# Performance work log

Hardware: AMD Instinct MI355X
Metric: run time of the kernel (lower is better)

Reference implementation:

```python
import jax, jax.numpy as jnp
import numpy as np

B, S, H, FF, E = 4, 4096, 1024, 4096, 8
EPS = 1e-5


def setup_inputs() -> dict:
    key = jax.random.key(0)
    ks = jax.random.split(key, 8)
    std = 0.02
    return {
        "x": jax.random.normal(ks[0], (B, S, H), jnp.float32),
        "norm_weight": jnp.ones((H,), jnp.float32),
        "router_w": jax.random.normal(ks[1], (E, H), jnp.float32) * std,
        "router_b": jnp.zeros((E,), jnp.float32),
        "fc1_w": jax.random.normal(ks[2], (E, FF, H), jnp.float32) * std,
        "fc1_b": jnp.zeros((E, FF), jnp.float32),
        "fc2_w": jax.random.normal(ks[3], (E, H, FF), jnp.float32) * std,
        "fc2_b": jnp.zeros((E, H), jnp.float32),
    }


def reference(x, norm_weight, router_w, router_b, fc1_w, fc1_b, fc2_w, fc2_b):
    b, s, h = x.shape
    T = b * s
    e = router_w.shape[0]
    cap = T // e  # expert capacity, capacity_factor = 1.0

    x_flat = x.reshape(T, h)
    # RMSNorm (pre-norm on MoE input)
    xn = x_flat * jax.lax.rsqrt(jnp.mean(x_flat * x_flat, axis=-1, keepdims=True) + EPS) * norm_weight

    # Router (no jitter: eval / jitter_noise=0)
    logits = xn @ router_w.T + router_b          # [T, E]
    probs = jax.nn.softmax(logits, axis=-1)       # [T, E]

    # Expert-choice routing: each expert picks its top-`cap` tokens by prob
    gates, idx = jax.lax.top_k(probs.T, cap)      # [E, cap], [E, cap]

    # Dispatch (gather) and grouped expert MLP
    xe = xn[idx]                                   # [E, cap, H]
    hmid = jnp.einsum('ech,efh->ecf', xe, fc1_w) + fc1_b[:, None, :]
    hmid = jax.nn.gelu(hmid, approximate=False)    # torch F.gelu default (exact)
    ye = jnp.einsum('ecf,ehf->ech', hmid, fc2_w) + fc2_b[:, None, :]

    # Combine: gated scatter-add back to token positions, normalize by gate sum
    flat_idx = idx.reshape(-1)                     # [E*cap]
    weighted = (ye * gates[..., None]).reshape(-1, h)
    out = jnp.zeros((T, h), x.dtype).at[flat_idx].add(weighted)
    gate_sums = jnp.zeros((T, 1), x.dtype).at[flat_idx].add(gates.reshape(-1, 1))
    out = out / jnp.maximum(gate_sums, 1e-9)       # unrouted tokens stay zero
    return out.reshape(b, s, h)
```

## Files before the change

### kernel.cpp

```cpp
#include <hip/hip_runtime.h>
#include <hip/hip_bf16.h>

#define T_TOK 16384
#define H_DIM 1024
#define FF_DIM 4096
#define NE 8
#define CAP 2048
#define EPS_F 1e-5f

#define BM2 256
#define BN2 256
#define BK2 32

typedef __attribute__((ext_vector_type(4))) float f32x4;
typedef __attribute__((ext_vector_type(8))) short bf16x8;
typedef unsigned long long u64;
typedef unsigned int u32;

__device__ inline void gload_lds16(const void* g, void* l) {
  __builtin_amdgcn_global_load_lds(
      (const __attribute__((address_space(1))) unsigned int*)g,
      (__attribute__((address_space(3))) unsigned int*)l, 16, 0, 0);
}

__device__ inline unsigned short bf16_bits(float f) {
  __hip_bfloat16 h = __float2bfloat16(f);
  unsigned short u;
  __builtin_memcpy(&u, &h, 2);
  return u;
}

__device__ inline float bits_f32(unsigned short u) {
  const u32 x = ((u32)u) << 16;
  float f;
  __builtin_memcpy(&f, &x, 4);
  return f;
}

__global__ __launch_bounds__(256) void router_kernel(
    const float* __restrict__ x, const float* __restrict__ nw,
    const float* __restrict__ rw, const float* __restrict__ rb,
    __hip_bfloat16* __restrict__ xn, u64* __restrict__ keys) {
  const int t = blockIdx.x;
  const int tid = threadIdx.x;
  const float4 v = reinterpret_cast<const float4*>(x + (size_t)t * H_DIM)[tid];
  float ss = v.x * v.x + v.y * v.y + v.z * v.z + v.w * v.w;
#pragma unroll
  for (int o = 32; o > 0; o >>= 1) ss += __shfl_down(ss, o);
  __shared__ float red[4];
  __shared__ float redl[4][NE];
  const int wv = tid >> 6, ln = tid & 63;
  if (ln == 0) red[wv] = ss;
  __syncthreads();
  const float tot = red[0] + red[1] + red[2] + red[3];
  const float scale = rsqrtf(tot * (1.0f / H_DIM) + EPS_F);
  const float4 w4 = reinterpret_cast<const float4*>(nw)[tid];
  float xv0 = v.x * scale * w4.x, xv1 = v.y * scale * w4.y;
  float xv2 = v.z * scale * w4.z, xv3 = v.w * scale * w4.w;
  ushort4 u4;
  u4.x = bf16_bits(xv0); u4.y = bf16_bits(xv1);
  u4.z = bf16_bits(xv2); u4.w = bf16_bits(xv3);
  reinterpret_cast<ushort4*>(xn + (size_t)t * H_DIM)[tid] = u4;
  float lg[NE];
#pragma unroll
  for (int e = 0; e < NE; ++e) {
    const float4 r4 = reinterpret_cast<const float4*>(rw + (size_t)e * H_DIM)[tid];
    lg[e] = xv0 * r4.x + xv1 * r4.y + xv2 * r4.z + xv3 * r4.w;
  }
#pragma unroll
  for (int o = 32; o > 0; o >>= 1) {
#pragma unroll
    for (int e = 0; e < NE; ++e) lg[e] += __shfl_down(lg[e], o);
  }
  if (ln == 0) {
#pragma unroll
    for (int e = 0; e < NE; ++e) redl[wv][e] = lg[e];
  }
  __syncthreads();
  if (tid == 0) {
    float l[NE];
    float m = -1e30f;
#pragma unroll
    for (int e = 0; e < NE; ++e) {
      l[e] = redl[0][e] + redl[1][e] + redl[2][e] + redl[3][e] + rb[e];
      m = fmaxf(m, l[e]);
    }
    float s = 0.f;
#pragma unroll
    for (int e = 0; e < NE; ++e) { l[e] = expf(l[e] - m); s += l[e]; }
    const float inv = 1.0f / s;
#pragma unroll
    for (int e = 0; e < NE; ++e) {
      const float p = l[e] * inv;
      const u64 key = ((u64)__float_as_uint(p) << 32) | (u32)(0xFFFFFFFFu - (u32)t);
      keys[(size_t)e * T_TOK + t] = key;
    }
  }
}

#define EQCAP 7168
__global__ __launch_bounds__(1024) void topk_kernel(
    const u64* __restrict__ keys, int* __restrict__ idxl,
    float* __restrict__ gatel, int* __restrict__ tok_list, int* __restrict__ tok_cnt) {
  const int e = blockIdx.x;
  const int tid = threadIdx.x;
  const int lane = tid & 63;
  const u64* ke = keys + (size_t)e * T_TOK;
  __shared__ int hist[256];
  __shared__ u32 s_pref;
  __shared__ int s_k;
  __shared__ int s_cnt;
  __shared__ int s_eq;
  __shared__ u32 eqlist[EQCAP];

  u32 pref = 0;
  int pbits = 0;
  int kneed = CAP;
  for (int pass = 0; pass < 4; ++pass) {
    if (tid < 256) hist[tid] = 0;
    __syncthreads();
    const int shift = 24 - 8 * pass;
    for (int i = tid; i < T_TOK; i += 1024) {
      const u32 hi = (u32)(ke[i] >> 32);
      const bool ok = (pbits == 0) || ((hi >> (32 - pbits)) == pref);
      const int d = ok ? (int)((hi >> shift) & 255) : -1;
      u64 act = __ballot(ok);
      while (act) {
        const int src = __ffsll((long long)act) - 1;
        const int dl = __shfl(d, src);
        const u64 mb = __ballot(ok && (d == dl));
        if (lane == src) atomicAdd(&hist[dl], (int)__popcll(mb));
        act &= ~mb;
      }
    }
    __syncthreads();
    if (tid == 0) {
      int cum = 0;
      int d = 255;
      for (; d >= 0; --d) {
        cum += hist[d];
        if (cum >= kneed) break;
      }
      s_k = kneed - (cum - hist[d]);
      s_pref = (pref << 8) | (u32)d;
    }
    __syncthreads();
    pref = s_pref;
    kneed = s_k;
    pbits += 8;
    __syncthreads();
  }
  const u32 thrp = pref;
  const float thrp_f = __uint_as_float(thrp);

  if (tid == 0) { s_cnt = 0; s_eq = 0; }
  __syncthreads();
  for (int i = tid; i < T_TOK; i += 1024) {
    const u64 key = ke[i];
    const u32 hi = (u32)(key >> 32);
    if (hi > thrp) {
      const int pos = atomicAdd(&s_cnt, 1);
      if (pos < CAP) {
        const int tok = (int)(0xFFFFFFFFu - (u32)key);
        idxl[e * CAP + pos] = tok;
        gatel[e * CAP + pos] = __uint_as_float(hi);
        const int j = atomicAdd(tok_cnt + tok, 1);
        if (j < NE) tok_list[tok * NE + j] = e * CAP + pos;
      }
    } else if (hi == thrp) {
      const int j = atomicAdd(&s_eq, 1);
      if (j < EQCAP) eqlist[j] = (u32)key;
    }
  }
  __syncthreads();
  const int neq = s_eq;
  if (neq <= EQCAP) {
    u32 prefl = 0;
    int pb = 0;
    int kn = kneed;
    if (neq > kneed) {
      for (int pass = 0; pass < 4; ++pass) {
        if (tid < 256) hist[tid] = 0;
        __syncthreads();
        const int shift = 24 - 8 * pass;
        for (int i = tid; i < neq; i += 1024) {
          const u32 vv = eqlist[i];
          if ((pb == 0) || ((vv >> (32 - pb)) == prefl)) atomicAdd(&hist[(vv >> shift) & 255], 1);
        }
        __syncthreads();
        if (tid == 0) {
          int cum = 0;
          int d = 255;
          for (; d >= 0; --d) {
            cum += hist[d];
            if (cum >= kn) break;
          }
          s_k = kn - (cum - hist[d]);
          s_pref = (prefl << 8) | (u32)d;
        }
        __syncthreads();
        prefl = s_pref;
        kn = s_k;
        pb += 8;
        __syncthreads();
      }
    }
    for (int i = tid; i < neq; i += 1024) {
      const u32 lo = eqlist[i];
      if (neq <= kneed || lo >= prefl) {
        const int pos = atomicAdd(&s_cnt, 1);
        if (pos < CAP) {
          const int tok = (int)(0xFFFFFFFFu - lo);
          idxl[e * CAP + pos] = tok;
          gatel[e * CAP + pos] = thrp_f;
          const int j = atomicAdd(tok_cnt + tok, 1);
          if (j < NE) tok_list[tok * NE + j] = e * CAP + pos;
        }
      }
    }
  } else {
    u64 pref64 = (u64)thrp;
    int pb64 = 32;
    int kn = kneed;
    for (int pass = 4; pass < 8; ++pass) {
      if (tid < 256) hist[tid] = 0;
      __syncthreads();
      const int shift = 56 - 8 * pass;
      for (int i = tid; i < T_TOK; i += 1024) {
        const u64 key = ke[i];
        if ((key >> (64 - pb64)) == pref64) atomicAdd(&hist[(int)((key >> shift) & 255)], 1);
      }
      __syncthreads();
      if (tid == 0) {
        int cum = 0;
        int d = 255;
        for (; d >= 0; --d) {
          cum += hist[d];
          if (cum >= kn) break;
        }
        s_k = kn - (cum - hist[d]);
        s_pref = (u32)d;
      }
      __syncthreads();
      pref64 = (pref64 << 8) | s_pref;
      kn = s_k;
      pb64 += 8;
      __syncthreads();
    }
    for (int i = tid; i < T_TOK; i += 1024) {
      const u64 key = ke[i];
      if ((u32)(key >> 32) == thrp && key >= pref64) {
        const int pos = atomicAdd(&s_cnt, 1);
        if (pos < CAP) {
          const int tok = (int)(0xFFFFFFFFu - (u32)key);
          idxl[e * CAP + pos] = tok;
          gatel[e * CAP + pos] = thrp_f;
          const int j = atomicAdd(tok_cnt + tok, 1);
          if (j < NE) tok_list[tok * NE + j] = e * CAP + pos;
        }
      }
    }
  }
}

template <int MODE>
__global__ __launch_bounds__(1024, 4) void gemm9_kernel(
    const __hip_bfloat16* __restrict__ Asrc, const float* __restrict__ Bw,
    const float* __restrict__ bias, const int* __restrict__ idxl,
    const float* __restrict__ gatel, __hip_bfloat16* __restrict__ hmid,
    __hip_bfloat16* __restrict__ ye, int ebase) {
  constexpr int N = (MODE == 0) ? FF_DIM : H_DIM;
  constexpr int K = (MODE == 0) ? H_DIM : FF_DIM;
  constexpr int NBN = N / BN2;
  constexpr int LOG_NBN = (MODE == 0) ? 4 : 2;
  constexpr int BPE = (CAP / BM2) * NBN;
  constexpr int LOG_BPE = (MODE == 0) ? 7 : 5;
  constexpr int NT = K / BK2;

  const int nwg = gridDim.x;
  const int wg0 = blockIdx.x;
  const int wg = (wg0 & 7) * (nwg >> 3) + (wg0 >> 3);
  const int z = wg >> LOG_BPE;
  const int rr = wg & (BPE - 1);
  const int bm = rr >> LOG_NBN;
  const int bn = rr & (NBN - 1);
  const int e = ebase + z;

  const int tid = threadIdx.x;
  const int lane = tid & 63;
  const int w = tid >> 6;
  const int wr = w >> 2, wc = w & 3;
  const int fr = lane & 15, q = lane >> 4;

  __shared__ char smem[147456];

  const int arow = tid >> 2;
  const int ag = tid & 3;
  const int askz = (ag ^ ((arow >> 1) & 3)) * 8;
  const __hip_bfloat16* asrc;
  if constexpr (MODE == 0) {
    const int t0 = idxl[e * CAP + bm * BM2 + arow];
    asrc = Asrc + (size_t)t0 * H_DIM + askz;
  } else {
    asrc = Asrc + ((size_t)z * CAP + bm * BM2 + arow) * FF_DIM + askz;
  }
  const int brow = tid >> 3;
  const int bg = tid & 7;
  const int bskz = (bg ^ (brow & 7)) * 4;
  const float* bsrc0 = Bw + (size_t)z * N * K + (size_t)(bn * BN2 + brow) * K + bskz;
  const float* bsrc1 = bsrc0 + (size_t)128 * K;

  f32x4 acc[4][4] = {};

#define STAGE9(sb, k0)                                   \
  do {                                                   \
    char* d_ = smem + (sb)*49152 + tid * 16;             \
    gload_lds16(asrc + (k0), d_);                        \
    gload_lds16(bsrc0 + (k0), d_ + 16384);               \
    gload_lds16(bsrc1 + (k0), d_ + 32768);               \
  } while (0)

  STAGE9(0, 0);
  STAGE9(1, BK2);
  STAGE9(2, 2 * BK2);
  asm volatile("s_waitcnt vmcnt(6)");
  __builtin_amdgcn_s_barrier();
  __builtin_amdgcn_sched_barrier(0);

  for (int kt = 0; kt < NT; ++kt) {
    const int sl = kt % 3;
    const char* base = smem + sl * 49152;
    bf16x8 Af[4], Bf[4];
#pragma unroll
    for (int m = 0; m < 4; ++m)
      Af[m] = *reinterpret_cast<const bf16x8*>(
          base + (wr * 64 + m * 16 + fr) * 64 + ((q ^ ((fr >> 1) & 3)) << 4));
#pragma unroll
    for (int n = 0; n < 4; ++n) {
      const int row = wc * 64 + n * 16 + fr;
      const char* rb = base + 16384 + row * 128;
      const float4 lo = *reinterpret_cast<const float4*>(rb + (((2 * q) ^ (row & 7)) << 4));
      const float4 hi = *reinterpret_cast<const float4*>(rb + (((2 * q + 1) ^ (row & 7)) << 4));
      bf16x8 f;
      f[0] = (short)bf16_bits(lo.x); f[1] = (short)bf16_bits(lo.y);
      f[2] = (short)bf16_bits(lo.z); f[3] = (short)bf16_bits(lo.w);
      f[4] = (short)bf16_bits(hi.x); f[5] = (short)bf16_bits(hi.y);
      f[6] = (short)bf16_bits(hi.z); f[7] = (short)bf16_bits(hi.w);
      Bf[n] = f;
    }
    asm volatile("s_waitcnt lgkmcnt(0)");
    __builtin_amdgcn_sched_barrier(0);
    __builtin_amdgcn_s_barrier();
    __builtin_amdgcn_sched_barrier(0);
    const int kref = (kt + 3 < NT) ? (kt + 3) : (kt + 3 - NT);
    STAGE9(sl, kref * BK2);
    asm volatile("s_waitcnt vmcnt(6)");
    __builtin_amdgcn_sched_barrier(0);
    __builtin_amdgcn_s_setprio(1);
#pragma unroll
    for (int m_ = 0; m_ < 4; ++m_)
#pragma unroll
      for (int n_ = 0; n_ < 4; ++n_)
        acc[m_][n_] = __builtin_amdgcn_mfma_f32_16x16x32_bf16(Af[m_], Bf[n_], acc[m_][n_], 0, 0, 0);
    __builtin_amdgcn_s_setprio(0);
    __builtin_amdgcn_s_barrier();
    __builtin_amdgcn_sched_barrier(0);
  }
#undef STAGE9

  if constexpr (MODE == 0) {
#pragma unroll
    for (int m = 0; m < 4; ++m) {
      const int rbase = bm * BM2 + wr * 64 + m * 16 + q * 4;
#pragma unroll
      for (int n = 0; n < 4; ++n) {
        const int gn = bn * BN2 + wc * 64 + n * 16 + fr;
        const float bb = bias[e * FF_DIM + gn];
#pragma unroll
        for (int i = 0; i < 4; ++i) {
          const float v = acc[m][n][i] + bb;
          const float u = v * (1.5957691216f + 0.0713548162972f * v * v);
          const float s = 1.0f / (1.0f + __expf(-u));
          hmid[((size_t)z * CAP + rbase + i) * FF_DIM + gn] = __float2bfloat16(v * s);
        }
      }
    }
  } else {
#pragma unroll
    for (int m = 0; m < 4; ++m) {
      const int rbase = bm * BM2 + wr * 64 + m * 16 + q * 4;
      float gt[4];
#pragma unroll
      for (int i = 0; i < 4; ++i) gt[i] = gatel[e * CAP + rbase + i];
#pragma unroll
      for (int n = 0; n < 4; ++n) {
        const int gn = bn * BN2 + wc * 64 + n * 16 + fr;
        const float bb = bias[e * H_DIM + gn];
#pragma unroll
        for (int i = 0; i < 4; ++i)
          ye[((size_t)e * CAP + rbase + i) * H_DIM + gn] =
              __float2bfloat16((acc[m][n][i] + bb) * gt[i]);
      }
    }
  }
}

__global__ __launch_bounds__(256) void combine_kernel(
    const __hip_bfloat16* __restrict__ ye, const float* __restrict__ gatel,
    const int* __restrict__ tok_list, const int* __restrict__ tok_cnt,
    float* __restrict__ out) {
  const int t = blockIdx.x;
  const int tid = threadIdx.x;
  const int cnt = tok_cnt[t];
  float a0 = 0.f, a1 = 0.f, a2 = 0.f, a3 = 0.f, gs = 0.f;
  for (int j = 0; j < cnt && j < NE; ++j) {
    const int ent = tok_list[t * NE + j];
    gs += gatel[ent];
    const ushort4 v = reinterpret_cast<const ushort4*>(ye + (size_t)ent * H_DIM)[tid];
    a0 += bits_f32(v.x);
    a1 += bits_f32(v.y);
    a2 += bits_f32(v.z);
    a3 += bits_f32(v.w);
  }
  const float inv = 1.0f / fmaxf(gs, 1e-9f);
  float4 o;
  o.x = a0 * inv; o.y = a1 * inv; o.z = a2 * inv; o.w = a3 * inv;
  reinterpret_cast<float4*>(out + (size_t)t * H_DIM)[tid] = o;
}

extern "C" void kernel_launch(void* const* d_in, const int* in_sizes, int n_in,
                              void* d_out, int out_size, void* d_ws, size_t ws_size,
                              hipStream_t stream) {
  const float* x = (const float*)d_in[0];
  const float* nw = (const float*)d_in[1];
  const float* rw = (const float*)d_in[2];
  const float* rb = (const float*)d_in[3];
  const float* fc1w = (const float*)d_in[4];
  const float* fc1b = (const float*)d_in[5];
  const float* fc2w = (const float*)d_in[6];
  const float* fc2b = (const float*)d_in[7];
  float* out = (float*)d_out;

  char* ws = (char*)d_ws;
  size_t off = 0;
  auto alloc = [&](size_t b) {
    char* p = ws + off;
    off += (b + 255) & ~(size_t)255;
    return p;
  };
  __hip_bfloat16* xn = (__hip_bfloat16*)alloc((size_t)T_TOK * H_DIM * 2);
  u64* keys = (u64*)alloc((size_t)NE * T_TOK * 8);
  int* idxl = (int*)alloc((size_t)NE * CAP * 4);
  float* gatel = (float*)alloc((size_t)NE * CAP * 4);
  int* tok_list = (int*)alloc((size_t)T_TOK * NE * 4);
  int* tok_cnt = (int*)alloc((size_t)T_TOK * 4);
  __hip_bfloat16* ye = (__hip_bfloat16*)alloc((size_t)NE * CAP * H_DIM * 2);

  int EC = NE;
  while (EC > 1) {
    const size_t per = (size_t)EC * (size_t)CAP * FF_DIM * 2;
    if (off + per + 4096 <= ws_size) break;
    EC >>= 1;
  }
  __hip_bfloat16* hmid = (__hip_bfloat16*)alloc((size_t)EC * CAP * FF_DIM * 2);

  hipMemsetAsync(tok_cnt, 0, (size_t)T_TOK * 4, stream);

  router_kernel<<<T_TOK, 256, 0, stream>>>(x, nw, rw, rb, xn, keys);
  topk_kernel<<<NE, 1024, 0, stream>>>(keys, idxl, gatel, tok_list, tok_cnt);

  for (int eb = 0; eb < NE; eb += EC) {
    const int nb1 = EC * (CAP / BM2) * (FF_DIM / BN2);
    gemm9_kernel<0><<<nb1, 1024, 0, stream>>>(xn, fc1w + (size_t)eb * FF_DIM * H_DIM, fc1b,
                                              idxl, gatel, hmid, ye, eb);
    const int nb2 = EC * (CAP / BM2) * (H_DIM / BN2);
    gemm9_kernel<1><<<nb2, 1024, 0, stream>>>(hmid, fc2w + (size_t)eb * H_DIM * FF_DIM, fc2b,
                                              idxl, gatel, hmid, ye, eb);
  }
  combine_kernel<<<T_TOK, 256, 0, stream>>>(ye, gatel, tok_list, tok_cnt, out);
}
```

Baseline: 629.7 us.

## Convert fp32 weights to bf16 once per tile in LDS and split MFMA phases

The GEMM main loop now reads fp32 weight rows into registers, converts them to bf16 once, and writes them into LDS. Previously every wave converted fp32 values read from LDS, duplicating the conversion work, and the fp32 staging used twice the LDS space. The loop is restructured into a 4-slot ring: A tiles arrive via direct global-to-LDS loads three tiles ahead, B tiles are register-prefetched two ahead, and the MFMA work is split into two halves around the convert-and-write step to overlap it. The token-count memset is folded into the router kernel. The pipeline adds register pressure and barrier/waitcnt subtleties that could introduce hazards.

```diff
diff --git a/kernel.cpp b/kernel.cpp
--- a/kernel.cpp
+++ b/kernel.cpp
@@ -40,9 +40,11 @@
 __global__ __launch_bounds__(256) void router_kernel(
     const float* __restrict__ x, const float* __restrict__ nw,
     const float* __restrict__ rw, const float* __restrict__ rb,
-    __hip_bfloat16* __restrict__ xn, u64* __restrict__ keys) {
+    __hip_bfloat16* __restrict__ xn, u64* __restrict__ keys,
+    int* __restrict__ tok_cnt) {
   const int t = blockIdx.x;
   const int tid = threadIdx.x;
+  if (tid == 0) tok_cnt[t] = 0;
   const float4 v = reinterpret_cast<const float4*>(x + (size_t)t * H_DIM)[tid];
   float ss = v.x * v.x + v.y * v.y + v.z * v.z + v.w * v.w;
 #pragma unroll
@@ -264,7 +266,7 @@
 }
 
 template <int MODE>
-__global__ __launch_bounds__(1024, 4) void gemm9_kernel(
+__global__ __launch_bounds__(1024) void gemm11_kernel(
     const __hip_bfloat16* __restrict__ Asrc, const float* __restrict__ Bw,
     const float* __restrict__ bias, const int* __restrict__ idxl,
     const float* __restrict__ gatel, __hip_bfloat16* __restrict__ hmid,
@@ -292,81 +294,111 @@
   const int wr = w >> 2, wc = w & 3;
   const int fr = lane & 15, q = lane >> 4;
 
-  __shared__ char smem[147456];
-
-  const int arow = tid >> 2;
-  const int ag = tid & 3;
-  const int askz = (ag ^ ((arow >> 1) & 3)) * 8;
+  __shared__ char smem[131072];
+
+  const int srow = tid >> 2;
+  const int sg = tid & 3;
+  const int skoff = (sg ^ ((srow >> 1) & 3)) * 8;
+
   const __hip_bfloat16* asrc;
   if constexpr (MODE == 0) {
-    const int t0 = idxl[e * CAP + bm * BM2 + arow];
-    asrc = Asrc + (size_t)t0 * H_DIM + askz;
+    const int t0 = idxl[e * CAP + bm * BM2 + srow];
+    asrc = Asrc + (size_t)t0 * H_DIM + skoff;
   } else {
-    asrc = Asrc + ((size_t)z * CAP + bm * BM2 + arow) * FF_DIM + askz;
-  }
-  const int brow = tid >> 3;
-  const int bg = tid & 7;
-  const int bskz = (bg ^ (brow & 7)) * 4;
-  const float* bsrc0 = Bw + (size_t)z * N * K + (size_t)(bn * BN2 + brow) * K + bskz;
-  const float* bsrc1 = bsrc0 + (size_t)128 * K;
+    asrc = Asrc + ((size_t)z * CAP + bm * BM2 + srow) * FF_DIM + skoff;
+  }
+  const float* bsrcf = Bw + (size_t)z * N * K + (size_t)(bn * BN2 + srow) * K + skoff;
+
+  const int slotk = ((q ^ ((fr >> 1) & 3)) << 4);
+  const int aoff0 = (wr * 64 + fr) * 64 + slotk;
+  const int boff0 = 16384 + (wc * 64 + fr) * 64 + slotk;
 
   f32x4 acc[4][4] = {};
-
-#define STAGE9(sb, k0)                                   \
-  do {                                                   \
-    char* d_ = smem + (sb)*49152 + tid * 16;             \
-    gload_lds16(asrc + (k0), d_);                        \
-    gload_lds16(bsrc0 + (k0), d_ + 16384);               \
-    gload_lds16(bsrc1 + (k0), d_ + 32768);               \
+  bf16x8 Af[4], Bf[4];
+  float4 bA0, bA1, bB0, bB1;
+
+#define GLDA(sb, k0) gload_lds16(asrc + (k0), smem + (sb)*32768 + tid * 16)
+#define CVT_WRITE(sl, c0, c1)                                               \
+  do {                                                                      \
+    bf16x8 wv_;                                                             \
+    wv_[0] = (short)bf16_bits((c0).x); wv_[1] = (short)bf16_bits((c0).y);   \
+    wv_[2] = (short)bf16_bits((c0).z); wv_[3] = (short)bf16_bits((c0).w);   \
+    wv_[4] = (short)bf16_bits((c1).x); wv_[5] = (short)bf16_bits((c1).y);   \
+    wv_[6] = (short)bf16_bits((c1).z); wv_[7] = (short)bf16_bits((c1).w);   \
+    *reinterpret_cast<bf16x8*>(smem + (sl)*32768 + 16384 + tid * 16) = wv_; \
   } while (0)
 
-  STAGE9(0, 0);
-  STAGE9(1, BK2);
-  STAGE9(2, 2 * BK2);
-  asm volatile("s_waitcnt vmcnt(6)");
+  GLDA(0, 0);
+  GLDA(1, BK2);
+  {
+    const float4 t0 = *reinterpret_cast<const float4*>(bsrcf);
+    const float4 t1 = *reinterpret_cast<const float4*>(bsrcf + 4);
+    CVT_WRITE(0, t0, t1);
+  }
+  __builtin_amdgcn_sched_barrier(0);
+  bA0 = *reinterpret_cast<const float4*>(bsrcf + BK2);
+  bA1 = *reinterpret_cast<const float4*>(bsrcf + BK2 + 4);
+  __builtin_amdgcn_sched_barrier(0);
+  GLDA(2, 2 * BK2);
+  __builtin_amdgcn_sched_barrier(0);
+  asm volatile("s_waitcnt lgkmcnt(0)");
   __builtin_amdgcn_s_barrier();
   __builtin_amdgcn_sched_barrier(0);
 
-  for (int kt = 0; kt < NT; ++kt) {
-    const int sl = kt % 3;
-    const char* base = smem + sl * 49152;
-    bf16x8 Af[4], Bf[4];
-#pragma unroll
-    for (int m = 0; m < 4; ++m)
-      Af[m] = *reinterpret_cast<const bf16x8*>(
-          base + (wr * 64 + m * 16 + fr) * 64 + ((q ^ ((fr >> 1) & 3)) << 4));
-#pragma unroll
-    for (int n = 0; n < 4; ++n) {
-      const int row = wc * 64 + n * 16 + fr;
-      const char* rb = base + 16384 + row * 128;
-      const float4 lo = *reinterpret_cast<const float4*>(rb + (((2 * q) ^ (row & 7)) << 4));
-      const float4 hi = *reinterpret_cast<const float4*>(rb + (((2 * q + 1) ^ (row & 7)) << 4));
-      bf16x8 f;
-      f[0] = (short)bf16_bits(lo.x); f[1] = (short)bf16_bits(lo.y);
-      f[2] = (short)bf16_bits(lo.z); f[3] = (short)bf16_bits(lo.w);
-      f[4] = (short)bf16_bits(hi.x); f[5] = (short)bf16_bits(hi.y);
-      f[6] = (short)bf16_bits(hi.z); f[7] = (short)bf16_bits(hi.w);
-      Bf[n] = f;
-    }
-    asm volatile("s_waitcnt lgkmcnt(0)");
-    __builtin_amdgcn_sched_barrier(0);
-    __builtin_amdgcn_s_barrier();
-    __builtin_amdgcn_sched_barrier(0);
-    const int kref = (kt + 3 < NT) ? (kt + 3) : (kt + 3 - NT);
-    STAGE9(sl, kref * BK2);
-    asm volatile("s_waitcnt vmcnt(6)");
-    __builtin_amdgcn_sched_barrier(0);
-    __builtin_amdgcn_s_setprio(1);
-#pragma unroll
-    for (int m_ = 0; m_ < 4; ++m_)
-#pragma unroll
-      for (int n_ = 0; n_ < 4; ++n_)
-        acc[m_][n_] = __builtin_amdgcn_mfma_f32_16x16x32_bf16(Af[m_], Bf[n_], acc[m_][n_], 0, 0, 0);
-    __builtin_amdgcn_s_setprio(0);
-    __builtin_amdgcn_s_barrier();
-    __builtin_amdgcn_sched_barrier(0);
-  }
-#undef STAGE9
+#define TILE(kt, c0, c1, n0, n1)                                                               \
+  {                                                                                            \
+    const int cur_ = (kt)&3;                                                                   \
+    const int psl_ = ((kt) + 3) & 3;                                                           \
+    const int bsl_ = ((kt) + 1) & 3;                                                           \
+    const int krA_ = ((kt) + 3 < NT) ? (kt) + 3 : (kt) + 3 - NT;                               \
+    const int krB_ = ((kt) + 2 < NT) ? (kt) + 2 : (kt) + 2 - NT;                               \
+    const char* base_ = smem + cur_ * 32768;                                                   \
+    Af[0] = *reinterpret_cast<const bf16x8*>(base_ + aoff0);                                   \
+    Af[1] = *reinterpret_cast<const bf16x8*>(base_ + aoff0 + 1024);                            \
+    Af[2] = *reinterpret_cast<const bf16x8*>(base_ + aoff0 + 2048);                            \
+    Af[3] = *reinterpret_cast<const bf16x8*>(base_ + aoff0 + 3072);                            \
+    Bf[0] = *reinterpret_cast<const bf16x8*>(base_ + boff0);                                   \
+    Bf[1] = *reinterpret_cast<const bf16x8*>(base_ + boff0 + 1024);                            \
+    __builtin_amdgcn_sched_barrier(0);                                                         \
+    Bf[2] = *reinterpret_cast<const bf16x8*>(base_ + boff0 + 2048);                            \
+    Bf[3] = *reinterpret_cast<const bf16x8*>(base_ + boff0 + 3072);                            \
+    n0 = *reinterpret_cast<const float4*>(bsrcf + krB_ * BK2);                                 \
+    n1 = *reinterpret_cast<const float4*>(bsrcf + krB_ * BK2 + 4);                             \
+    __builtin_amdgcn_sched_barrier(0);                                                         \
+    GLDA(psl_, krA_ * BK2);                                                                    \
+    __builtin_amdgcn_sched_barrier(0);                                                         \
+    asm volatile("s_waitcnt vmcnt(6)");          \
+    __builtin_amdgcn_s_barrier();                                                              \
+    asm volatile("s_waitcnt lgkmcnt(2)");                             \
+    __builtin_amdgcn_sched_barrier(0);                                                         \
+    __builtin_amdgcn_s_setprio(1);                                                             \
+    _Pragma("unroll") for (int m_ = 0; m_ < 4; ++m_) {                                         \
+      acc[m_][0] = __builtin_amdgcn_mfma_f32_16x16x32_bf16(Af[m_], Bf[0], acc[m_][0], 0, 0, 0);\
+      acc[m_][1] = __builtin_amdgcn_mfma_f32_16x16x32_bf16(Af[m_], Bf[1], acc[m_][1], 0, 0, 0);\
+    }                                                                                          \
+    __builtin_amdgcn_s_setprio(0);                                                             \
+    __builtin_amdgcn_sched_barrier(0);                                                         \
+    CVT_WRITE(bsl_, c0, c1);              \
+    asm volatile("s_waitcnt lgkmcnt(0)");                                                      \
+    __builtin_amdgcn_sched_barrier(0);                                                         \
+    __builtin_amdgcn_s_barrier();                                                              \
+    __builtin_amdgcn_sched_barrier(0);                                                         \
+    __builtin_amdgcn_s_setprio(1);                                                             \
+    _Pragma("unroll") for (int m_ = 0; m_ < 4; ++m_) {                                         \
+      acc[m_][2] = __builtin_amdgcn_mfma_f32_16x16x32_bf16(Af[m_], Bf[2], acc[m_][2], 0, 0, 0);\
+      acc[m_][3] = __builtin_amdgcn_mfma_f32_16x16x32_bf16(Af[m_], Bf[3], acc[m_][3], 0, 0, 0);\
+    }                                                                                          \
+    __builtin_amdgcn_s_setprio(0);                                                             \
+    __builtin_amdgcn_sched_barrier(0);                                                         \
+  }
+
+  for (int kt = 0; kt < NT; kt += 2) {
+    TILE(kt, bA0, bA1, bB0, bB1);
+    TILE(kt + 1, bB0, bB1, bA0, bA1);
+  }
+#undef TILE
+#undef GLDA
+#undef CVT_WRITE
 
   if constexpr (MODE == 0) {
 #pragma unroll
@@ -464,18 +496,16 @@
   }
   __hip_bfloat16* hmid = (__hip_bfloat16*)alloc((size_t)EC * CAP * FF_DIM * 2);
 
-  hipMemsetAsync(tok_cnt, 0, (size_t)T_TOK * 4, stream);
-
-  router_kernel<<<T_TOK, 256, 0, stream>>>(x, nw, rw, rb, xn, keys);
+  router_kernel<<<T_TOK, 256, 0, stream>>>(x, nw, rw, rb, xn, keys, tok_cnt);
   topk_kernel<<<NE, 1024, 0, stream>>>(keys, idxl, gatel, tok_list, tok_cnt);
 
   for (int eb = 0; eb < NE; eb += EC) {
     const int nb1 = EC * (CAP / BM2) * (FF_DIM / BN2);
-    gemm9_kernel<0><<<nb1, 1024, 0, stream>>>(xn, fc1w + (size_t)eb * FF_DIM * H_DIM, fc1b,
-                                              idxl, gatel, hmid, ye, eb);
+    gemm11_kernel<0><<<nb1, 1024, 0, stream>>>(xn, fc1w + (size_t)eb * FF_DIM * H_DIM, fc1b,
+                                               idxl, gatel, hmid, ye, eb);
     const int nb2 = EC * (CAP / BM2) * (H_DIM / BN2);
-    gemm9_kernel<1><<<nb2, 1024, 0, stream>>>(hmid, fc2w + (size_t)eb * H_DIM * FF_DIM, fc2b,
-                                              idxl, gatel, hmid, ye, eb);
+    gemm11_kernel<1><<<nb2, 1024, 0, stream>>>(hmid, fc2w + (size_t)eb * H_DIM * FF_DIM, fc2b,
+                                               idxl, gatel, hmid, ye, eb);
   }
   combine_kernel<<<T_TOK, 256, 0, stream>>>(ye, gatel, tok_list, tok_cnt, out);
 }
```

New measurement: 647.7 us. 2.9% more time.
